# Optimization experiments

Measured on AMD Instinct MI355X. Metric: run time of the kernel, lower is better.

## Reference

```python
import jax, jax.numpy as jnp
import numpy as np

N_NODES = 50000
N_EDGES = 800000
N_GRAPHS = 16
F_IN = 128
E_DIM = 16
HID = 32
HEADS = 2
EPS_BN = 1e-5


def gatv2_conv(x, edge_index, edge_attr, Wl, bl, Wr, br, We, att, bias, heads, out_ch):
    """PyG GATv2Conv (share_weights=False, concat=True, add_self_loops=True, fill_value='mean')."""
    n = x.shape[0]
    src, dst = edge_index[0], edge_index[1]
    loop = jnp.arange(n)
    src = jnp.concatenate([src, loop])
    dst = jnp.concatenate([dst, loop])
    ea = jnp.concatenate([edge_attr, jnp.broadcast_to(edge_attr.mean(0), (n, edge_attr.shape[1]))])
    x_l = (x @ Wl + bl).reshape(n, heads, out_ch)   # source transform
    x_r = (x @ Wr + br).reshape(n, heads, out_ch)   # target transform
    e = (ea @ We).reshape(-1, heads, out_ch)
    m = jax.nn.leaky_relu(x_l[src] + x_r[dst] + e, 0.2)      # [E, H, C]
    alpha = (m * att[None]).sum(-1)                          # [E, H]
    amax = jax.ops.segment_max(alpha, dst, num_segments=n)
    ex = jnp.exp(alpha - amax[dst])
    denom = jax.ops.segment_sum(ex, dst, num_segments=n)
    alpha = ex / (denom[dst] + 1e-16)
    out = jax.ops.segment_sum(x_l[src] * alpha[..., None], dst, num_segments=n)
    return out.reshape(n, heads * out_ch) + bias


def batch_norm(x, g, b):
    mu = x.mean(0)
    var = jnp.var(x, axis=0)  # biased, as torch BatchNorm1d training mode
    return (x - mu) * jax.lax.rsqrt(var + EPS_BN) * g + b


def setup_inputs() -> dict:
    key = jax.random.key(0)
    ks = jax.random.split(key, 24)
    s = 0.1
    d1 = HID * HEADS  # 64
    inp = {
        'x': jax.random.normal(ks[0], (N_NODES, F_IN), jnp.float32),
        'edge_index': jax.random.randint(ks[1], (2, N_EDGES), 0, N_NODES),
        'edge_attr': jax.random.normal(ks[2], (N_EDGES, E_DIM), jnp.float32),
        'batch': jnp.sort(jax.random.randint(ks[3], (N_NODES,), 0, N_GRAPHS)),
        'skip1_W': jax.random.normal(ks[4], (F_IN, d1)) * s,
        'skip1_b': jnp.zeros((d1,)),
        'conv1_Wl': jax.random.normal(ks[5], (F_IN, d1)) * s,
        'conv1_bl': jnp.zeros((d1,)),
        'conv1_Wr': jax.random.normal(ks[6], (F_IN, d1)) * s,
        'conv1_br': jnp.zeros((d1,)),
        'conv1_We': jax.random.normal(ks[7], (E_DIM, d1)) * s,
        'conv1_att': jax.random.normal(ks[8], (HEADS, HID)) * s,
        'conv1_bias': jnp.zeros((d1,)),
        'bn1_g': jnp.ones((d1,)),
        'bn1_b': jnp.zeros((d1,)),
        'skip2_W': jax.random.normal(ks[9], (d1, HID)) * s,
        'skip2_b': jnp.zeros((HID,)),
        'conv2_Wl': jax.random.normal(ks[10], (d1, HID)) * s,
        'conv2_bl': jnp.zeros((HID,)),
        'conv2_Wr': jax.random.normal(ks[11], (d1, HID)) * s,
        'conv2_br': jnp.zeros((HID,)),
        'conv2_We': jax.random.normal(ks[12], (E_DIM, HID)) * s,
        'conv2_att': jax.random.normal(ks[13], (1, HID)) * s,
        'conv2_bias': jnp.zeros((HID,)),
        'bn2_g': jnp.ones((HID,)),
        'bn2_b': jnp.zeros((HID,)),
    }
    return inp


def reference(x, edge_index, edge_attr, batch,
              skip1_W, skip1_b, conv1_Wl, conv1_bl, conv1_Wr, conv1_br, conv1_We, conv1_att, conv1_bias, bn1_g, bn1_b,
              skip2_W, skip2_b, conv2_Wl, conv2_bl, conv2_Wr, conv2_br, conv2_We, conv2_att, conv2_bias, bn2_g, bn2_b):
    h_proj = x @ skip1_W + skip1_b
    h = gatv2_conv(x, edge_index, edge_attr, conv1_Wl, conv1_bl, conv1_Wr, conv1_br, conv1_We, conv1_att, conv1_bias, HEADS, HID)
    h = jax.nn.elu(batch_norm(h, bn1_g, bn1_b) + h_proj)
    h_proj = h @ skip2_W + skip2_b
    h2 = gatv2_conv(h, edge_index, edge_attr, conv2_Wl, conv2_bl, conv2_Wr, conv2_br, conv2_We, conv2_att, conv2_bias, 1, HID)
    h2 = jax.nn.elu(batch_norm(h2, bn2_g, bn2_b) + h_proj)
    ones = jnp.ones((h2.shape[0],), h2.dtype)
    counts = jax.ops.segment_sum(ones, batch, num_segments=N_GRAPHS)
    x_mean = jax.ops.segment_sum(h2, batch, num_segments=N_GRAPHS) / jnp.maximum(counts, 1.0)[:, None]
    x_max = jax.ops.segment_max(h2, batch, num_segments=N_GRAPHS)
    x_max = jnp.where(counts[:, None] > 0, x_max, 0.0)
    return jnp.concatenate([x_mean, x_max], axis=1)
```

## Files before the change

kernel.cpp:

```cpp
#include <hip/hip_runtime.h>
#include <hip/hip_bf16.h>

#define NE 800000
#define NN 50000
#define NG 16
#define ETOT (NE + NN)

typedef unsigned short u16;
typedef __attribute__((ext_vector_type(8))) short short8;
typedef __attribute__((ext_vector_type(4))) float float4v;

__device__ __forceinline__ float b2f(u16 u) {
  return __uint_as_float(((unsigned)u) << 16);
}
__device__ __forceinline__ u16 f2b(float f) {
  __hip_bfloat16 b = __float2bfloat16(f);
  return *(u16*)&b;
}
__device__ __forceinline__ void cv8(uint4 v, float* o) {
  o[0] = __uint_as_float(v.x << 16);
  o[1] = __uint_as_float(v.x & 0xFFFF0000u);
  o[2] = __uint_as_float(v.y << 16);
  o[3] = __uint_as_float(v.y & 0xFFFF0000u);
  o[4] = __uint_as_float(v.z << 16);
  o[5] = __uint_as_float(v.z & 0xFFFF0000u);
  o[6] = __uint_as_float(v.w << 16);
  o[7] = __uint_as_float(v.w & 0xFFFF0000u);
}
__device__ __forceinline__ unsigned pk2(float a, float b) {
  return (unsigned)f2b(a) | ((unsigned)f2b(b) << 16);
}
__device__ __forceinline__ unsigned f2key(float f) {
  unsigned u = __float_as_uint(f);
  return (u & 0x80000000u) ? ~u : (u | 0x80000000u);
}
__device__ __forceinline__ float key2f(unsigned k) {
  unsigned u = (k & 0x80000000u) ? (k ^ 0x80000000u) : ~k;
  return __uint_as_float(u);
}
__device__ __forceinline__ int plaus(unsigned h) {
  unsigned eh = (h >> 7) & 0xFF;
  return (h == 0) || (eh >= 100 && eh <= 140);
}
__device__ __forceinline__ float lrelu(float v) {
  return (v > 0.f) ? v : 0.2f * v;
}

__global__ __launch_bounds__(256) void k_init(uint4* __restrict__ zbase, int zcnt16,
                                              const unsigned* __restrict__ a,
                                              const unsigned* __restrict__ b,
                                              const unsigned* __restrict__ c,
                                              int* __restrict__ flags) {
  uint4 z = {0, 0, 0, 0};
  for (int i = blockIdx.x * 256 + threadIdx.x; i < zcnt16; i += gridDim.x * 256)
    zbase[i] = z;
  if (blockIdx.x != 0) return;
  __shared__ int cnt[3];
  if (threadIdx.x < 3) cnt[threadIdx.x] = 0;
  __syncthreads();
  const unsigned* arr[3] = {a, b, c};
  for (int k = 0; k < 3; k++) {
    int ok = 0;
    for (int i = threadIdx.x; i < 4096; i += 256) {
      unsigned w = arr[k][i];
      ok += (plaus(w & 0xFFFFu) && plaus(w >> 16)) ? 1 : 0;
    }
    atomicAdd(&cnt[k], ok);
  }
  __syncthreads();
  if (threadIdx.x == 0) {
    int f0 = cnt[0] > 2048, f1 = cnt[1] > 2048, f2 = cnt[2] > 2048;
    flags[0] = f0;
    flags[1] = f1;
    flags[2] = f2;
    flags[3] = f0 && f1 && f2;
  }
}

__global__ __launch_bounds__(256) void k_histcol(const int* __restrict__ ei,
                                                 const void* __restrict__ ea,
                                                 const void* __restrict__ xin,
                                                 const int* __restrict__ flg,
                                                 int* __restrict__ deg4,
                                                 float* __restrict__ mean_part,
                                                 u16* __restrict__ xh,
                                                 u16* __restrict__ xlo) {
  int gt = blockIdx.x * 256 + threadIdx.x;
  if (gt < ETOT) {
    int dst = (gt < NE) ? ei[NE + gt] : gt - NE;
    atomicAdd(&deg4[(blockIdx.x & 3) * NN + dst], 1);
  }
  bool eb = flg[2] != 0;
  int col = gt & 15;
  int row = gt >> 4;
  int rstride = (gridDim.x * 256) >> 4;
  float s = 0.f;
  if (eb) {
    const u16* p = (const u16*)ea;
    for (int e = row; e < NE; e += rstride) s += b2f(p[(size_t)e * 16 + col]);
  } else {
    const float* p = (const float*)ea;
    for (int e = row; e < NE; e += rstride) s += p[(size_t)e * 16 + col];
  }
  __shared__ float ls[256];
  ls[threadIdx.x] = s;
  __syncthreads();
  if (threadIdx.x < 16) {
    float t = 0.f;
    for (int i = threadIdx.x; i < 256; i += 16) t += ls[i];
    atomicAdd(&mean_part[(blockIdx.x & 63) * 16 + threadIdx.x], t);
  }
  if (flg[0] == 0) {
    const float4* xp4 = (const float4*)xin;
    const int nch = NN * 32;
    int stride = gridDim.x * 256;
    for (int i = gt; i < nch; i += stride) {
      float4 v = xp4[i];
      u16 h0 = f2b(v.x), h1 = f2b(v.y), h2 = f2b(v.z), h3 = f2b(v.w);
      u16 l0 = f2b(v.x - b2f(h0));
      u16 l1 = f2b(v.y - b2f(h1));
      u16 l2 = f2b(v.z - b2f(h2));
      u16 l3 = f2b(v.w - b2f(h3));
      uint2 ho, lo2;
      ho.x = (unsigned)h0 | ((unsigned)h1 << 16);
      ho.y = (unsigned)h2 | ((unsigned)h3 << 16);
      lo2.x = (unsigned)l0 | ((unsigned)l1 << 16);
      lo2.y = (unsigned)l2 | ((unsigned)l3 << 16);
      *(uint2*)(xh + (size_t)i * 4) = ho;
      *(uint2*)(xlo + (size_t)i * 4) = lo2;
    }
  }
}

template <int K, int N, int RPB>
__device__ __forceinline__ void gemm_direct(
    const void* __restrict__ W, const void* __restrict__ bb, bool wb,
    const u16* __restrict__ xh, const u16* __restrict__ xlo, bool has_lo,
    u16* __restrict__ out, int tile) {
  constexpr int CT = N / 16;
  constexpr int WPC = 4 / CT;
  constexpr int KK = K / 32;
  int lane = threadIdx.x & 63;
  int wave = threadIdx.x >> 6;
  int col = lane & 15;
  int quad = lane >> 4;
  int ct = wave % CT;
  int rt_off = wave / CT;
  short8 bh[KK], bl[KK];
#pragma unroll
  for (int kk = 0; kk < KK; kk++) {
    short8 th, tl;
#pragma unroll
    for (int j = 0; j < 8; j++) {
      int k = kk * 32 + quad * 8 + j;
      float w = wb ? b2f(((const u16*)W)[k * N + ct * 16 + col])
                   : ((const float*)W)[k * N + ct * 16 + col];
      u16 hb = f2b(w);
      th[j] = (short)hb;
      tl[j] = (short)f2b(w - b2f(hb));
    }
    bh[kk] = th;
    bl[kk] = tl;
  }
  float bias = wb ? b2f(((const u16*)bb)[ct * 16 + col])
                  : ((const float*)bb)[ct * 16 + col];
  int rt0 = tile * RPB;
  for (int i = rt_off; i < RPB; i += WPC) {
    int rt = rt0 + i;
    int row = rt * 16 + col;
    float4v acc = {0.f, 0.f, 0.f, 0.f};
#pragma unroll
    for (int kk = 0; kk < KK; kk++) {
      short8 afh = *(const short8*)(xh + (size_t)row * K + kk * 32 + quad * 8);
      acc = __builtin_amdgcn_mfma_f32_16x16x32_bf16(afh, bh[kk], acc, 0, 0, 0);
      if (has_lo) {
        short8 afl = *(const short8*)(xlo + (size_t)row * K + kk * 32 + quad * 8);
        acc = __builtin_amdgcn_mfma_f32_16x16x32_bf16(afl, bh[kk], acc, 0, 0, 0);
      }
      if (!wb)
        acc = __builtin_amdgcn_mfma_f32_16x16x32_bf16(afh, bl[kk], acc, 0, 0, 0);
    }
#pragma unroll
    for (int r = 0; r < 4; r++) {
      int orow = rt * 16 + quad * 4 + r;
      out[(size_t)orow * N + ct * 16 + col] = f2b(acc[r] + bias);
    }
  }
}

template <int K, int N, int TILES, int RPB>
__global__ __launch_bounds__(256) void k_scanlin1(
    const int* __restrict__ deg4, int* __restrict__ start, int* __restrict__ cursor,
    const float* __restrict__ mean_part, float* __restrict__ mean_sums,
    const void* __restrict__ xin, const u16* __restrict__ xh,
    const u16* __restrict__ xlo, const int* __restrict__ flg,
    const void* W0, const void* W1, const void* W2,
    const void* b0, const void* b1, const void* b2,
    u16* __restrict__ o0, u16* __restrict__ o1, u16* __restrict__ o2, int M) {
  (void)M;
  __shared__ __align__(16) int smem[512];

  if ((int)blockIdx.x == 0) {
    int t = threadIdx.x;
    if (t < 16) {
      float s = 0.f;
#pragma unroll
      for (int j = 0; j < 64; j++) s += mean_part[j * 16 + t];
      mean_sums[t] = s;
    }
    constexpr int NT = (NN + 1023) / 1024;
    int* ws = smem;
    int* tbase = ws + 256;
    int lane = t & 63;
    int wv = t >> 6;
    for (int tile = 0; tile < NT; tile++) {
      int idx = tile * 1024 + t * 4;
      int4 d = {0, 0, 0, 0};
      if (idx + 3 < NN) {
#pragma unroll
        for (int c = 0; c < 4; c++) {
          int4 dc = *(const int4*)(deg4 + c * NN + idx);
          d.x += dc.x; d.y += dc.y; d.z += dc.z; d.w += dc.w;
        }
      } else {
#pragma unroll
        for (int c = 0; c < 4; c++) {
          if (idx + 0 < NN) d.x += deg4[c * NN + idx + 0];
          if (idx + 1 < NN) d.y += deg4[c * NN + idx + 1];
          if (idx + 2 < NN) d.z += deg4[c * NN + idx + 2];
          if (idx + 3 < NN) d.w += deg4[c * NN + idx + 3];
        }
      }
      int s4 = d.x + d.y + d.z + d.w;
      int r = s4;
#pragma unroll
      for (int ofs = 1; ofs < 64; ofs <<= 1) r += __shfl_xor(r, ofs, 64);
      if (lane == 0) ws[tile * 4 + wv] = r;
    }
    __syncthreads();
    if (wv == 0) {
      int g0 = 0, g1 = 0, g2 = 0, g3 = 0;
      if (lane < NT) {
        g0 = ws[lane * 4 + 0];
        g1 = ws[lane * 4 + 1];
        g2 = ws[lane * 4 + 2];
        g3 = ws[lane * 4 + 3];
      }
      int gs = g0 + g1 + g2 + g3;
      int sc = gs;
#pragma unroll
      for (int ofs = 1; ofs < 64; ofs <<= 1) {
        int v = __shfl_up(sc, ofs, 64);
        if (lane >= ofs) sc += v;
      }
      int base = sc - gs;
      if (lane < NT) {
        tbase[lane * 4 + 0] = base;
        tbase[lane * 4 + 1] = base + g0;
        tbase[lane * 4 + 2] = base + g0 + g1;
        tbase[lane * 4 + 3] = base + g0 + g1 + g2;
      }
      if (lane == NT - 1) start[NN] = base + gs;
    }
    __syncthreads();
    for (int tile = 0; tile < NT; tile++) {
      int idx = tile * 1024 + t * 4;
      int4 d = {0, 0, 0, 0};
      if (idx + 3 < NN) {
#pragma unroll
        for (int c = 0; c < 4; c++) {
          int4 dc = *(const int4*)(deg4 + c * NN + idx);
          d.x += dc.x; d.y += dc.y; d.z += dc.z; d.w += dc.w;
        }
      } else {
#pragma unroll
        for (int c = 0; c < 4; c++) {
          if (idx + 0 < NN) d.x += deg4[c * NN + idx + 0];
          if (idx + 1 < NN) d.y += deg4[c * NN + idx + 1];
          if (idx + 2 < NN) d.z += deg4[c * NN + idx + 2];
          if (idx + 3 < NN) d.w += deg4[c * NN + idx + 3];
        }
      }
      int s4 = d.x + d.y + d.z + d.w;
      int sc = s4;
#pragma unroll
      for (int ofs = 1; ofs < 64; ofs <<= 1) {
        int v = __shfl_up(sc, ofs, 64);
        if (lane >= ofs) sc += v;
      }
      int excl = tbase[tile * 4 + wv] + (sc - s4);
      int4 st;
      st.x = excl;
      st.y = excl + d.x;
      st.z = st.y + d.y;
      st.w = st.z + d.z;
      if (idx + 3 < NN) {
        *(int4*)(start + idx) = st;
        *(int4*)(cursor + idx) = st;
      } else {
        if (idx + 0 < NN) { start[idx + 0] = st.x; cursor[idx + 0] = st.x; }
        if (idx + 1 < NN) { start[idx + 1] = st.y; cursor[idx + 1] = st.y; }
        if (idx + 2 < NN) { start[idx + 2] = st.z; cursor[idx + 2] = st.z; }
        if (idx + 3 < NN) { start[idx + 3] = st.w; cursor[idx + 3] = st.w; }
      }
    }
    return;
  }
  int lidx = blockIdx.x - 1;
  int wset = lidx / TILES;
  int tile = lidx % TILES;
  bool wb = flg[1] != 0;
  bool xb = flg[0] != 0;
  const void* W = wset == 0 ? W0 : (wset == 1 ? W1 : W2);
  const void* bb = wset == 0 ? b0 : (wset == 1 ? b1 : b2);
  u16* out = wset == 0 ? o0 : (wset == 1 ? o1 : o2);
  const u16* ah = xb ? (const u16*)xin : xh;
  gemm_direct<K, N, RPB>(W, bb, wb, ah, xlo, !xb, out, tile);
}

__global__ __launch_bounds__(256) void k_buildcsr_pay(
    const int* __restrict__ ei, const void* __restrict__ eattr,
    const int* __restrict__ flg, const float* __restrict__ mean_sums,
    int* __restrict__ cursor, int* __restrict__ csr_src,
    u16* __restrict__ ea16) {
  int e = blockIdx.x * 256 + threadIdx.x;
  if (e >= ETOT) return;
  bool eb = flg[2] != 0;
  int src, dst;
  if (e < NE) { src = ei[e]; dst = ei[NE + e]; } else { src = dst = e - NE; }
  float rec[16];
  if (e < NE) {
    if (eb) {
      const uint4* q = (const uint4*)((const u16*)eattr + (size_t)e * 16);
      cv8(q[0], rec);
      cv8(q[1], rec + 8);
    } else {
      const float* q = (const float*)eattr + (size_t)e * 16;
#pragma unroll
      for (int k = 0; k < 16; k++) rec[k] = q[k];
    }
  } else {
#pragma unroll
    for (int k = 0; k < 16; k++) rec[k] = mean_sums[k] * (1.0f / NE);
  }
  int pos = atomicAdd(&cursor[dst], 1);
  csr_src[pos] = src;
  u16 rb[16];
#pragma unroll
  for (int k = 0; k < 16; k++) rb[k] = f2b(rec[k]);
  uint4* dp = (uint4*)(ea16 + (size_t)pos * 16);
  dp[0] = *(uint4*)rb;
  dp[1] = *(uint4*)(rb + 8);
}

__global__ __launch_bounds__(256) void k_buildcsr(const int* __restrict__ ei,
                                                  int* __restrict__ cursor,
                                                  uint2* __restrict__ csr) {
  int e = blockIdx.x * 256 + threadIdx.x;
  if (e >= ETOT) return;
  int src, dst;
  if (e < NE) { src = ei[e]; dst = ei[NE + e]; } else { src = dst = e - NE; }
  int pos = atomicAdd(&cursor[dst], 1);
  uint2 r; r.x = (unsigned)src; r.y = (unsigned)e;
  csr[pos] = r;
}

__global__ __launch_bounds__(256) void k_ewgemm(
    const u16* __restrict__ ea, const int* __restrict__ flg,
    const void* We1, const void* We2,
    u16* __restrict__ ew1, u16* __restrict__ ew2) {
  bool wb = flg[1] != 0;
  int lane = threadIdx.x & 63;
  int col = lane & 15;
  int quad = lane >> 4;
  short8 b1h[4], b1l[4], b2h[2], b2l[2];
#pragma unroll
  for (int ct = 0; ct < 4; ct++) {
    short8 th, tl;
#pragma unroll
    for (int j = 0; j < 8; j++) {
      int k = quad * 8 + j;
      float w = 0.f;
      if (k < 16)
        w = wb ? b2f(((const u16*)We1)[k * 64 + ct * 16 + col])
               : ((const float*)We1)[k * 64 + ct * 16 + col];
      u16 hb = f2b(w);
      th[j] = (short)hb;
      tl[j] = (short)f2b(w - b2f(hb));
    }
    b1h[ct] = th; b1l[ct] = tl;
  }
#pragma unroll
  for (int ct = 0; ct < 2; ct++) {
    short8 th, tl;
#pragma unroll
    for (int j = 0; j < 8; j++) {
      int k = quad * 8 + j;
      float w = 0.f;
      if (k < 16)
        w = wb ? b2f(((const u16*)We2)[k * 32 + ct * 16 + col])
               : ((const float*)We2)[k * 32 + ct * 16 + col];
      u16 hb = f2b(w);
      th[j] = (short)hb;
      tl[j] = (short)f2b(w - b2f(hb));
    }
    b2h[ct] = th; b2l[ct] = tl;
  }
  int nw = (gridDim.x * 256) >> 6;
  int wid = (blockIdx.x * 256 + threadIdx.x) >> 6;
  const int NT = ETOT / 16;
  for (int rt = wid; rt < NT; rt += nw) {
    int row = rt * 16 + col;
    short8 af = {0, 0, 0, 0, 0, 0, 0, 0};
    if (quad < 2) af = *(const short8*)(ea + (size_t)row * 16 + quad * 8);
#pragma unroll
    for (int ct = 0; ct < 4; ct++) {
      float4v acc = {0.f, 0.f, 0.f, 0.f};
      acc = __builtin_amdgcn_mfma_f32_16x16x32_bf16(af, b1h[ct], acc, 0, 0, 0);
      acc = __builtin_amdgcn_mfma_f32_16x16x32_bf16(af, b1l[ct], acc, 0, 0, 0);
#pragma unroll
      for (int r = 0; r < 4; r++)
        ew1[(size_t)(rt * 16 + quad * 4 + r) * 64 + ct * 16 + col] = f2b(acc[r]);
    }
#pragma unroll
    for (int ct = 0; ct < 2; ct++) {
      float4v acc = {0.f, 0.f, 0.f, 0.f};
      acc = __builtin_amdgcn_mfma_f32_16x16x32_bf16(af, b2h[ct], acc, 0, 0, 0);
      acc = __builtin_amdgcn_mfma_f32_16x16x32_bf16(af, b2l[ct], acc, 0, 0, 0);
#pragma unroll
      for (int r = 0; r < 4; r++)
        ew2[(size_t)(rt * 16 + quad * 4 + r) * 32 + ct * 16 + col] = f2b(acc[r]);
    }
  }
}

template <int K, int N, int RPB>
__global__ __launch_bounds__(256) void k_lin3b(
    const void* __restrict__ xin, const int* __restrict__ flg,
    const void* W0, const void* W1, const void* W2,
    const void* b0, const void* b1, const void* b2,
    u16* __restrict__ o0, u16* __restrict__ o1, u16* __restrict__ o2, int M) {
  (void)M;
  bool wb = flg[1] != 0;
  const void* W = blockIdx.y == 0 ? W0 : (blockIdx.y == 1 ? W1 : W2);
  const void* bb = blockIdx.y == 0 ? b0 : (blockIdx.y == 1 ? b1 : b2);
  u16* out = blockIdx.y == 0 ? o0 : (blockIdx.y == 1 ? o1 : o2);
  gemm_direct<K, N, RPB>(W, bb, wb, (const u16*)xin, nullptr, false, out,
                         blockIdx.x);
}

__device__ __forceinline__ float dot16b(const u16* __restrict__ p,
                                        const float* __restrict__ W) {
  float ea[16];
  const uint4* q = (const uint4*)p;
  cv8(q[0], ea);
  cv8(q[1], ea + 8);
  float s = 0.f;
#pragma unroll
  for (int k = 0; k < 16; k++) s += ea[k] * W[k];
  return s;
}
__device__ __forceinline__ float dot16u(const u16* __restrict__ p,
                                        const float* __restrict__ W) {
  const uint4* q = (const uint4*)p;
  uint4 A = q[0], B = q[1];
  unsigned w0 = (unsigned)__builtin_amdgcn_readfirstlane((int)A.x);
  unsigned w1 = (unsigned)__builtin_amdgcn_readfirstlane((int)A.y);
  unsigned w2 = (unsigned)__builtin_amdgcn_readfirstlane((int)A.z);
  unsigned w3 = (unsigned)__builtin_amdgcn_readfirstlane((int)A.w);
  unsigned w4 = (unsigned)__builtin_amdgcn_readfirstlane((int)B.x);
  unsigned w5 = (unsigned)__builtin_amdgcn_readfirstlane((int)B.y);
  unsigned w6 = (unsigned)__builtin_amdgcn_readfirstlane((int)B.z);
  unsigned w7 = (unsigned)__builtin_amdgcn_readfirstlane((int)B.w);
  float s = 0.f;
  s += __uint_as_float(w0 << 16) * W[0];
  s += __uint_as_float(w0 & 0xFFFF0000u) * W[1];
  s += __uint_as_float(w1 << 16) * W[2];
  s += __uint_as_float(w1 & 0xFFFF0000u) * W[3];
  s += __uint_as_float(w2 << 16) * W[4];
  s += __uint_as_float(w2 & 0xFFFF0000u) * W[5];
  s += __uint_as_float(w3 << 16) * W[6];
  s += __uint_as_float(w3 & 0xFFFF0000u) * W[7];
  s += __uint_as_float(w4 << 16) * W[8];
  s += __uint_as_float(w4 & 0xFFFF0000u) * W[9];
  s += __uint_as_float(w5 << 16) * W[10];
  s += __uint_as_float(w5 & 0xFFFF0000u) * W[11];
  s += __uint_as_float(w6 << 16) * W[12];
  s += __uint_as_float(w6 & 0xFFFF0000u) * W[13];
  s += __uint_as_float(w7 << 16) * W[14];
  s += __uint_as_float(w7 & 0xFFFF0000u) * W[15];
  return s;
}
__device__ __forceinline__ float dot16f(const float* __restrict__ q,
                                        const float* __restrict__ W) {
  float s = 0.f;
#pragma unroll
  for (int k = 0; k < 16; k++) s += q[k] * W[k];
  return s;
}

template <int H, int C, bool PRE>
__global__ __launch_bounds__(256) void k_fusedp(
    const int* __restrict__ start, const int* __restrict__ csr_src,
    const u16* __restrict__ pay, const u16* __restrict__ ewp,
    const int* __restrict__ flg,
    const u16* __restrict__ xl, const u16* __restrict__ xr,
    const void* We, const void* att, u16* __restrict__ agg) {
  constexpr int D = H * C;
  constexpr int NPW = 64 / D;
  bool wb = flg[1] != 0;
  int lane = threadIdx.x & 63;
  int ch = lane % D;
  float Wreg[16];
  if constexpr (!PRE) {
    if (wb) {
      const u16* Wp = (const u16*)We;
#pragma unroll
      for (int k = 0; k < 16; k++) Wreg[k] = b2f(Wp[k * D + ch]);
    } else {
      const float* Wp = (const float*)We;
#pragma unroll
      for (int k = 0; k < 16; k++) Wreg[k] = Wp[k * D + ch];
    }
  }
  float attv = wb ? b2f(((const u16*)att)[ch]) : ((const float*)att)[ch];
  int wid = (blockIdx.x * 256 + threadIdx.x) >> 6;

  if constexpr (NPW == 1) {
    int node = __builtin_amdgcn_readfirstlane(wid);
    int s0 = __builtin_amdgcn_readfirstlane(start[node]);
    int s1 = __builtin_amdgcn_readfirstlane(start[node + 1]);
    float xrv = b2f(xr[(unsigned)node * D + ch]);
    float ssum = 0.f, acc = 0.f;
    int p = s0;
    for (; p + 3 < s1; p += 4) {
      int c0 = __builtin_amdgcn_readfirstlane(csr_src[p + 0]);
      int c1 = __builtin_amdgcn_readfirstlane(csr_src[p + 1]);
      int c2 = __builtin_amdgcn_readfirstlane(csr_src[p + 2]);
      int c3 = __builtin_amdgcn_readfirstlane(csr_src[p + 3]);
      float xlv0 = b2f(xl[(unsigned)c0 * D + ch]);
      float xlv1 = b2f(xl[(unsigned)c1 * D + ch]);
      float xlv2 = b2f(xl[(unsigned)c2 * D + ch]);
      float xlv3 = b2f(xl[(unsigned)c3 * D + ch]);
      float ev0, ev1, ev2, ev3;
      if constexpr (PRE) {
        ev0 = b2f(ewp[(size_t)(p + 0) * D + ch]);
        ev1 = b2f(ewp[(size_t)(p + 1) * D + ch]);
        ev2 = b2f(ewp[(size_t)(p + 2) * D + ch]);
        ev3 = b2f(ewp[(size_t)(p + 3) * D + ch]);
      } else {
        ev0 = dot16u(pay + (size_t)(p + 0) * 16, Wreg);
        ev1 = dot16u(pay + (size_t)(p + 1) * 16, Wreg);
        ev2 = dot16u(pay + (size_t)(p + 2) * 16, Wreg);
        ev3 = dot16u(pay + (size_t)(p + 3) * 16, Wreg);
      }
      float t0 = lrelu(xlv0 + xrv + ev0) * attv;
      float t1 = lrelu(xlv1 + xrv + ev1) * attv;
      float t2 = lrelu(xlv2 + xrv + ev2) * attv;
      float t3 = lrelu(xlv3 + xrv + ev3) * attv;
#pragma unroll
      for (int mk = 1; mk <= 16; mk <<= 1) {
        t0 += __shfl_xor(t0, mk, 64);
        t1 += __shfl_xor(t1, mk, 64);
        t2 += __shfl_xor(t2, mk, 64);
        t3 += __shfl_xor(t3, mk, 64);
      }
      float ex0 = __expf(t0);
      float ex1 = __expf(t1);
      float ex2 = __expf(t2);
      float ex3 = __expf(t3);
      ssum += (ex0 + ex1) + (ex2 + ex3);
      acc += ex0 * xlv0 + ex1 * xlv1;
      acc += ex2 * xlv2 + ex3 * xlv3;
    }
    for (; p < s1; ++p) {
      int c0 = __builtin_amdgcn_readfirstlane(csr_src[p]);
      float xlv = b2f(xl[(unsigned)c0 * D + ch]);
      float ev;
      if constexpr (PRE) ev = b2f(ewp[(size_t)p * D + ch]);
      else ev = dot16u(pay + (size_t)p * 16, Wreg);
      float t = lrelu(xlv + xrv + ev) * attv;
#pragma unroll
      for (int mk = 1; mk <= 16; mk <<= 1) t += __shfl_xor(t, mk, 64);
      float ex = __expf(t);
      ssum += ex;
      acc += ex * xlv;
    }
    agg[(size_t)node * D + ch] = f2b(acc / (ssum + 1e-16f));
  } else {
    int node = wid * NPW + lane / D;
    int s0 = start[node], s1 = start[node + 1];
    int deg = s1 - s0;
    int last = s1 - 1;
    int degmax = max(deg, __shfl_xor(deg, 32, 64));
    float xrv = b2f(xr[(unsigned)node * D + ch]);
    float ssum = 0.f, acc = 0.f;
    for (int i = 0; i < degmax; i += 4) {
      int p0 = min(s0 + i + 0, last);
      int p1 = min(s0 + i + 1, last);
      int p2 = min(s0 + i + 2, last);
      int p3 = min(s0 + i + 3, last);
      bool a0 = i + 0 < deg, a1 = i + 1 < deg, a2 = i + 2 < deg, a3 = i + 3 < deg;
      int c0 = csr_src[p0];
      int c1 = csr_src[p1];
      int c2 = csr_src[p2];
      int c3 = csr_src[p3];
      float xlv0 = b2f(xl[(unsigned)c0 * D + ch]);
      float xlv1 = b2f(xl[(unsigned)c1 * D + ch]);
      float xlv2 = b2f(xl[(unsigned)c2 * D + ch]);
      float xlv3 = b2f(xl[(unsigned)c3 * D + ch]);
      float ev0, ev1, ev2, ev3;
      if constexpr (PRE) {
        ev0 = b2f(ewp[(size_t)p0 * D + ch]);
        ev1 = b2f(ewp[(size_t)p1 * D + ch]);
        ev2 = b2f(ewp[(size_t)p2 * D + ch]);
        ev3 = b2f(ewp[(size_t)p3 * D + ch]);
      } else {
        ev0 = dot16b(pay + (size_t)p0 * 16, Wreg);
        ev1 = dot16b(pay + (size_t)p1 * 16, Wreg);
        ev2 = dot16b(pay + (size_t)p2 * 16, Wreg);
        ev3 = dot16b(pay + (size_t)p3 * 16, Wreg);
      }
      float t0 = lrelu(xlv0 + xrv + ev0) * attv;
      float t1 = lrelu(xlv1 + xrv + ev1) * attv;
      float t2 = lrelu(xlv2 + xrv + ev2) * attv;
      float t3 = lrelu(xlv3 + xrv + ev3) * attv;
#pragma unroll
      for (int mk = 1; mk <= 16; mk <<= 1) {
        t0 += __shfl_xor(t0, mk, 64);
        t1 += __shfl_xor(t1, mk, 64);
        t2 += __shfl_xor(t2, mk, 64);
        t3 += __shfl_xor(t3, mk, 64);
      }
      float ex0 = a0 ? __expf(t0) : 0.f;
      float ex1 = a1 ? __expf(t1) : 0.f;
      float ex2 = a2 ? __expf(t2) : 0.f;
      float ex3 = a3 ? __expf(t3) : 0.f;
      ssum += (ex0 + ex1) + (ex2 + ex3);
      acc += ex0 * xlv0 + ex1 * xlv1;
      acc += ex2 * xlv2 + ex3 * xlv3;
    }
    agg[(size_t)node * D + ch] = f2b(acc / (ssum + 1e-16f));
  }
}

template <int H, int C>
__global__ __launch_bounds__(256) void k_fusedg(
    const int* __restrict__ start, const uint2* __restrict__ csr,
    const void* __restrict__ eattr, const int* __restrict__ flg,
    const float* __restrict__ mean_sums,
    const u16* __restrict__ xl, const u16* __restrict__ xr,
    const void* We, const void* att, u16* __restrict__ agg) {
  constexpr int D = H * C;
  constexpr int NPW = 64 / D;
  bool wb = flg[1] != 0;
  bool eb = flg[2] != 0;
  int lane = threadIdx.x & 63;
  int ch = lane % D;
  float Wreg[16];
  if (wb) {
    const u16* Wp = (const u16*)We;
#pragma unroll
    for (int k = 0; k < 16; k++) Wreg[k] = b2f(Wp[k * D + ch]);
  } else {
    const float* Wp = (const float*)We;
#pragma unroll
    for (int k = 0; k < 16; k++) Wreg[k] = Wp[k * D + ch];
  }
  float attv = wb ? b2f(((const u16*)att)[ch]) : ((const float*)att)[ch];
  float ev_self = 0.f;
#pragma unroll
  for (int k = 0; k < 16; k++) ev_self += mean_sums[k] * (1.0f / NE) * Wreg[k];
  int wid = (blockIdx.x * 256 + threadIdx.x) >> 6;
  int node = wid * NPW + lane / D;
  int s0 = start[node], s1 = start[node + 1];
  int deg = s1 - s0;
  int last = s1 - 1;
  int degmax = deg;
  if constexpr (NPW == 2) degmax = max(deg, __shfl_xor(deg, 32, 64));
  float xrv = b2f(xr[(size_t)node * D + ch]);
  float ssum = 0.f, acc = 0.f;
  for (int i = 0; i < degmax; i += 2) {
    uint2 cr0 = csr[min(s0 + i, last)];
    uint2 cr1 = csr[min(s0 + i + 1, last)];
    bool a0 = i < deg, a1 = i + 1 < deg;
    float xlv0 = b2f(xl[(size_t)cr0.x * D + ch]);
    float xlv1 = b2f(xl[(size_t)cr1.x * D + ch]);
    float ev0 = cr0.y < NE ? (eb ? dot16b((const u16*)eattr + (size_t)cr0.y * 16, Wreg)
                                 : dot16f((const float*)eattr + (size_t)cr0.y * 16, Wreg))
                           : ev_self;
    float ev1 = cr1.y < NE ? (eb ? dot16b((const u16*)eattr + (size_t)cr1.y * 16, Wreg)
                                 : dot16f((const float*)eattr + (size_t)cr1.y * 16, Wreg))
                           : ev_self;
    float mv0 = xlv0 + xrv + ev0;
    float mv1 = xlv1 + xrv + ev1;
    mv0 = (mv0 > 0.f) ? mv0 : 0.2f * mv0;
    mv1 = (mv1 > 0.f) ? mv1 : 0.2f * mv1;
    float t0 = mv0 * attv, t1 = mv1 * attv;
#pragma unroll
    for (int mk = 1; mk <= 16; mk <<= 1) {
      t0 += __shfl_xor(t0, mk, 64);
      t1 += __shfl_xor(t1, mk, 64);
    }
    float ex0 = a0 ? __expf(t0) : 0.f;
    float ex1 = a1 ? __expf(t1) : 0.f;
    ssum += ex0 + ex1;
    acc += ex0 * xlv0 + ex1 * xlv1;
  }
  agg[(size_t)node * D + ch] = f2b(acc / (ssum + 1e-16f));
}

template <int D>
__global__ __launch_bounds__(256) void k_bnred(const u16* __restrict__ v,
                                               float* __restrict__ sum,
                                               float* __restrict__ sq, int M) {
  constexpr int RB = 256 / D;
  int tid = threadIdx.x;
  int c = tid % D;
  int rg = tid / D;
  float s = 0.f, q = 0.f;
  for (int r = blockIdx.x * RB + rg; r < M; r += gridDim.x * RB) {
    float x = b2f(v[(size_t)r * D + c]);
    s += x;
    q += x * x;
  }
  __shared__ float ls[256], lq[256];
  ls[tid] = s; lq[tid] = q;
  __syncthreads();
  if (tid < D) {
    float ts = 0.f, tq = 0.f;
    for (int i = tid; i < 256; i += D) { ts += ls[i]; tq += lq[i]; }
    atomicAdd(&sum[tid], ts);
    atomicAdd(&sq[tid], tq);
  }
}

template <int D>
__global__ __launch_bounds__(256) void k_bnapply(const u16* __restrict__ agg,
                                                 const u16* __restrict__ hp,
                                                 const float* __restrict__ sum,
                                                 const float* __restrict__ sq,
                                                 const void* g, const void* b,
                                                 const int* __restrict__ flg,
                                                 u16* __restrict__ out, int M) {
  bool wb = flg[1] != 0;
  int idx = blockIdx.x * 256 + threadIdx.x;
  if (idx >= M * D) return;
  int c = idx & (D - 1);
  float gc = wb ? b2f(((const u16*)g)[c]) : ((const float*)g)[c];
  float bc = wb ? b2f(((const u16*)b)[c]) : ((const float*)b)[c];
  float mu = sum[c] * (1.f / M);
  float var = fmaxf(sq[c] * (1.f / M) - mu * mu, 0.f);
  float sc = rsqrtf(var + 1e-5f) * gc;
  float v = (b2f(agg[idx]) - mu) * sc + bc + b2f(hp[idx]);
  v = v > 0.f ? v : expm1f(v);
  out[idx] = f2b(v);
}

__global__ __launch_bounds__(256) void k_poolall(
    const u16* __restrict__ agg2, const u16* __restrict__ hp2,
    const float* __restrict__ sum, const float* __restrict__ sq,
    const void* g, const void* b, const int* __restrict__ flg,
    const int* __restrict__ batch,
    float* __restrict__ pool_sum, unsigned* __restrict__ pool_maxk,
    float* __restrict__ pool_cnt, int* __restrict__ done_cnt,
    void* __restrict__ out) {
  bool wb = flg[1] != 0;
  int c = threadIdx.x & 31;
  int rg = threadIdx.x >> 5;
  float gc = wb ? b2f(((const u16*)g)[c]) : ((const float*)g)[c];
  float bc = wb ? b2f(((const u16*)b)[c]) : ((const float*)b)[c];
  float mu = sum[c] * (1.f / NN);
  float var = fmaxf(sq[c] * (1.f / NN) - mu * mu, 0.f);
  float scl = rsqrtf(var + 1e-5f) * gc;
  float sh = bc - mu * scl;

  const int NPB = 256;
  int n0 = blockIdx.x * NPB;
  int nend = min(n0 + NPB, NN);
  int cur = -1;
  float s = 0.f, mx = 0.f;
  int cnt = 0;
  for (int n = n0 + rg; n < nend; n += 8) {
    int gi = batch[n];
    float v = b2f(agg2[(size_t)n * 32 + c]) * scl + sh + b2f(hp2[(size_t)n * 32 + c]);
    v = v > 0.f ? v : expm1f(v);
    if (gi != cur) {
      if (cur >= 0) {
        atomicAdd(&pool_sum[cur * 32 + c], s);
        atomicMax(&pool_maxk[cur * 32 + c], f2key(mx));
        if (c == 0) atomicAdd(&pool_cnt[cur], (float)cnt);
      }
      cur = gi; s = 0.f; mx = -INFINITY; cnt = 0;
    }
    s += v;
    mx = fmaxf(mx, v);
    cnt++;
  }
  if (cur >= 0) {
    atomicAdd(&pool_sum[cur * 32 + c], s);
    atomicMax(&pool_maxk[cur * 32 + c], f2key(mx));
    if (c == 0) atomicAdd(&pool_cnt[cur], (float)cnt);
  }
  __threadfence();
  __syncthreads();
  __shared__ int lastblk;
  if (threadIdx.x == 0) lastblk = (atomicAdd(done_cnt, 1) == (int)gridDim.x - 1);
  __syncthreads();
  if (!lastblk) return;
  bool ob = flg[3] != 0;
  for (int idx = threadIdx.x; idx < NG * 64; idx += 256) {
    int gi = idx / 64, cc = idx % 64;
    float cntv = atomicAdd(&pool_cnt[gi], 0.f);
    float val;
    if (cc < 32) val = atomicAdd(&pool_sum[gi * 32 + cc], 0.f) / fmaxf(cntv, 1.f);
    else {
      unsigned k = atomicMax(&pool_maxk[gi * 32 + (cc - 32)], 0u);
      val = cntv > 0.f ? key2f(k) : 0.f;
    }
    if (ob) ((u16*)out)[idx] = f2b(val);
    else ((float*)out)[idx] = val;
  }
}

extern "C" void kernel_launch(void* const* d_in, const int* in_sizes, int n_in,
                              void* d_out, int out_size, void* d_ws, size_t ws_size,
                              hipStream_t stream) {
  (void)in_sizes; (void)n_in; (void)out_size;
  const void* x     = d_in[0];
  const int*  ei    = (const int*)d_in[1];
  const void* eattr = d_in[2];
  const int*  batch = (const int*)d_in[3];
  const void* skip1_W = d_in[4];
  const void* skip1_b = d_in[5];
  const void* c1_Wl = d_in[6];
  const void* c1_bl = d_in[7];
  const void* c1_Wr = d_in[8];
  const void* c1_br = d_in[9];
  const void* c1_We = d_in[10];
  const void* c1_att = d_in[11];
  const void* bn1_g = d_in[13];
  const void* bn1_b = d_in[14];
  const void* skip2_W = d_in[15];
  const void* skip2_b = d_in[16];
  const void* c2_Wl = d_in[17];
  const void* c2_bl = d_in[18];
  const void* c2_Wr = d_in[19];
  const void* c2_br = d_in[20];
  const void* c2_We = d_in[21];
  const void* c2_att = d_in[22];
  const void* bn2_g = d_in[24];
  const void* bn2_b = d_in[25];

  float* ws = (float*)d_ws;
  size_t off = 0;
  auto alloc = [&](size_t nfl) {
    float* p = ws + off;
    off += (nfl + 15) & ~(size_t)15;
    return p;
  };
  int*   flags      = (int*)alloc(16);
  float* mean_sums  = alloc(16);
  float* mean_part  = alloc(64 * 16);
  int*   deg4       = (int*)alloc((size_t)4 * NN);
  float* bnsum1     = alloc(64);
  float* bnsq1      = alloc(64);
  float* bnsum2     = alloc(32);
  float* bnsq2      = alloc(32);
  float* pool_cnt   = alloc(NG);
  float* pool_sum   = alloc(NG * 32);
  unsigned* pool_maxk = (unsigned*)alloc(NG * 32);
  int*   done_pool  = (int*)alloc(16);
  size_t zcnt16 = (off * sizeof(float)) / 16;
  u16* xh  = (u16*)alloc((size_t)NN * 64);
  u16* xlo = (u16*)alloc((size_t)NN * 64);
  size_t zoff = off;

  int* start   = (int*)alloc(NN + 1);
  int* cursor  = (int*)alloc(NN);
  int* csr_src = (int*)alloc(ETOT);
  u16* ea16    = (u16*)alloc((size_t)ETOT * 8);
  u16* ew1     = (u16*)alloc((size_t)ETOT * 32);
  u16* ew2     = (u16*)alloc((size_t)ETOT * 16);
  uint2* csr = nullptr;
  u16* xl1 = (u16*)alloc((size_t)NN * 32);
  u16* xr1 = (u16*)alloc((size_t)NN * 32);
  u16* hp1 = (u16*)alloc((size_t)NN * 32);
  u16* agg = (u16*)alloc((size_t)NN * 32);
  int tier = 0;
  if (off * sizeof(float) > ws_size) {
    tier = 1;
    off = zoff;
    start   = (int*)alloc(NN + 1);
    cursor  = (int*)alloc(NN);
    csr_src = (int*)alloc(ETOT);
    ea16    = (u16*)alloc((size_t)ETOT * 8);
    ew1 = ew2 = nullptr;
    xl1 = (u16*)alloc((size_t)NN * 32);
    xr1 = (u16*)alloc((size_t)NN * 32);
    hp1 = (u16*)alloc((size_t)NN * 32);
    agg = (u16*)alloc((size_t)NN * 32);
  }
  if (tier == 1 && off * sizeof(float) > ws_size) {
    tier = 2;
    off = zoff;
    start   = (int*)alloc(NN + 1);
    cursor  = (int*)alloc(NN);
    csr     = (uint2*)alloc((size_t)ETOT * 2);
    ea16    = nullptr;
    xl1 = (u16*)alloc((size_t)NN * 32);
    xr1 = (u16*)alloc((size_t)NN * 32);
    hp1 = (u16*)alloc((size_t)NN * 32);
    agg = (u16*)alloc((size_t)NN * 32);
  }
  u16* h1  = xr1;
  u16* xl2 = xl1;
  u16* xr2 = xl1 + (size_t)NN * 32;
  u16* hp2 = hp1;

  int eg = (ETOT + 255) / 256;

  k_init<<<128, 256, 0, stream>>>((uint4*)d_ws, (int)zcnt16,
                                  (const unsigned*)x, (const unsigned*)skip1_W,
                                  (const unsigned*)eattr, flags);
  k_histcol<<<eg, 256, 0, stream>>>(ei, eattr, x, flags, deg4, mean_part, xh, xlo);
  k_scanlin1<128, 64, 625, 5><<<1876, 256, 0, stream>>>(
      deg4, start, cursor, mean_part, mean_sums, x, xh, xlo, flags,
      c1_Wl, c1_Wr, skip1_W, c1_bl, c1_br, skip1_b, xl1, xr1, hp1, NN);
  if (tier <= 1) {
    k_buildcsr_pay<<<eg, 256, 0, stream>>>(ei, eattr, flags, mean_sums,
                                           cursor, csr_src, ea16);
  } else {
    k_buildcsr<<<eg, 256, 0, stream>>>(ei, cursor, csr);
  }
  if (tier == 0) {
    k_ewgemm<<<1024, 256, 0, stream>>>(ea16, flags, c1_We, c2_We, ew1, ew2);
  }
  if (tier == 0) {
    k_fusedp<2, 32, true><<<NN / 4, 256, 0, stream>>>(start, csr_src, ea16, ew1,
                                                      flags, xl1, xr1, c1_We,
                                                      c1_att, agg);
  } else if (tier == 1) {
    k_fusedp<2, 32, false><<<NN / 4, 256, 0, stream>>>(start, csr_src, ea16, nullptr,
                                                       flags, xl1, xr1, c1_We,
                                                       c1_att, agg);
  } else {
    k_fusedg<2, 32><<<NN / 4, 256, 0, stream>>>(start, csr, eattr, flags, mean_sums,
                                                xl1, xr1, c1_We, c1_att, agg);
  }
  k_bnred<64><<<256, 256, 0, stream>>>(agg, bnsum1, bnsq1, NN);
  k_bnapply<64><<<(NN * 64 + 255) / 256, 256, 0, stream>>>(agg, hp1, bnsum1, bnsq1,
                                                           bn1_g, bn1_b, flags, h1, NN);
  {
    dim3 g(625, 3);
    k_lin3b<64, 32, 5><<<g, 256, 0, stream>>>(h1, flags, c2_Wl, c2_Wr, skip2_W,
                                              c2_bl, c2_br, skip2_b,
                                              xl2, xr2, hp2, NN);
  }
  if (tier == 0) {
    k_fusedp<1, 32, true><<<NN / 8, 256, 0, stream>>>(start, csr_src, ea16, ew2,
                                                      flags, xl2, xr2, c2_We,
                                                      c2_att, agg);
  } else if (tier == 1) {
    k_fusedp<1, 32, false><<<NN / 8, 256, 0, stream>>>(start, csr_src, ea16, nullptr,
                                                       flags, xl2, xr2, c2_We,
                                                       c2_att, agg);
  } else {
    k_fusedg<1, 32><<<NN / 8, 256, 0, stream>>>(start, csr, eattr, flags, mean_sums,
                                                xl2, xr2, c2_We, c2_att, agg);
  }
  k_bnred<32><<<256, 256, 0, stream>>>(agg, bnsum2, bnsq2, NN);
  k_poolall<<<(NN + 255) / 256, 256, 0, stream>>>(agg, hp2, bnsum2, bnsq2,
                                                  bn2_g, bn2_b, flags, batch,
                                                  pool_sum, pool_maxk, pool_cnt,
                                                  done_pool, d_out);
}
```

Before: 589.7 us.

## Split single-block CSR prefix scan into parallel two-pass scan kernels

The degree prefix scan used to run serially inside block 0 of the fused scan+linear kernel, walking about 49 tiles of 1024 nodes twice. It now runs as two grid-wide kernels: one computes per-tile totals (and the edge-attr mean sums), the other scans those totals and writes start/cursor for each tile. The linear GEMM becomes its own kernel. This removes the long serial tail from block 0 at the cost of two extra launches and one more pass over deg4.

```diff
diff --git a/kernel.cpp b/kernel.cpp
--- a/kernel.cpp
+++ b/kernel.cpp
@@ -132,6 +132,114 @@
   }
 }
 
+#define SCAN_NT ((NN + 1023) / 1024)
+
+__global__ __launch_bounds__(256) void k_scansum(const int* __restrict__ deg4,
+                                                 const float* __restrict__ mean_part,
+                                                 float* __restrict__ mean_sums,
+                                                 int* __restrict__ tile_tot) {
+  int t = threadIdx.x;
+  if (blockIdx.x == 0 && t < 16) {
+    float s = 0.f;
+#pragma unroll
+    for (int j = 0; j < 64; j++) s += mean_part[j * 16 + t];
+    mean_sums[t] = s;
+  }
+  int lane = t & 63;
+  int wv = t >> 6;
+  int idx = blockIdx.x * 1024 + t * 4;
+  int s4 = 0;
+  if (idx + 3 < NN) {
+#pragma unroll
+    for (int c = 0; c < 4; c++) {
+      int4 dc = *(const int4*)(deg4 + c * NN + idx);
+      s4 += dc.x + dc.y + dc.z + dc.w;
+    }
+  } else {
+#pragma unroll
+    for (int c = 0; c < 4; c++) {
+      if (idx + 0 < NN) s4 += deg4[c * NN + idx + 0];
+      if (idx + 1 < NN) s4 += deg4[c * NN + idx + 1];
+      if (idx + 2 < NN) s4 += deg4[c * NN + idx + 2];
+      if (idx + 3 < NN) s4 += deg4[c * NN + idx + 3];
+    }
+  }
+  int r = s4;
+#pragma unroll
+  for (int ofs = 1; ofs < 64; ofs <<= 1) r += __shfl_xor(r, ofs, 64);
+  __shared__ int wsum[4];
+  if (lane == 0) wsum[wv] = r;
+  __syncthreads();
+  if (t == 0) tile_tot[blockIdx.x] = wsum[0] + wsum[1] + wsum[2] + wsum[3];
+}
+
+__global__ __launch_bounds__(256) void k_scanwrite(const int* __restrict__ deg4,
+                                                   const int* __restrict__ tile_tot,
+                                                   int* __restrict__ start,
+                                                   int* __restrict__ cursor) {
+  __shared__ int sbase;
+  __shared__ int wsum[4];
+  int t = threadIdx.x;
+  int lane = t & 63;
+  int wv = t >> 6;
+  if (wv == 0) {
+    int v = (lane < SCAN_NT) ? tile_tot[lane] : 0;
+    int sc = v;
+#pragma unroll
+    for (int ofs = 1; ofs < 64; ofs <<= 1) {
+      int u = __shfl_up(sc, ofs, 64);
+      if (lane >= ofs) sc += u;
+    }
+    if (lane == (int)blockIdx.x) sbase = sc - v;
+    if (blockIdx.x == 0 && lane == SCAN_NT - 1) start[NN] = sc;
+  }
+  int idx = blockIdx.x * 1024 + t * 4;
+  int4 d = {0, 0, 0, 0};
+  if (idx + 3 < NN) {
+#pragma unroll
+    for (int c = 0; c < 4; c++) {
+      int4 dc = *(const int4*)(deg4 + c * NN + idx);
+      d.x += dc.x; d.y += dc.y; d.z += dc.z; d.w += dc.w;
+    }
+  } else {
+#pragma unroll
+    for (int c = 0; c < 4; c++) {
+      if (idx + 0 < NN) d.x += deg4[c * NN + idx + 0];
+      if (idx + 1 < NN) d.y += deg4[c * NN + idx + 1];
+      if (idx + 2 < NN) d.z += deg4[c * NN + idx + 2];
+      if (idx + 3 < NN) d.w += deg4[c * NN + idx + 3];
+    }
+  }
+  int s4 = d.x + d.y + d.z + d.w;
+  int sc = s4;
+#pragma unroll
+  for (int ofs = 1; ofs < 64; ofs <<= 1) {
+    int v = __shfl_up(sc, ofs, 64);
+    if (lane >= ofs) sc += v;
+  }
+  if (lane == 63) wsum[wv] = sc;
+  __syncthreads();
+  int wbase = 0;
+#pragma unroll
+  for (int w = 0; w < 4; w++)
+    if (w < wv) wbase += wsum[w];
+  int excl = sbase + wbase + (sc - s4);
+  int4 st;
+  st.x = excl;
+  st.y = excl + d.x;
+  st.z = st.y + d.y;
+  st.w = st.z + d.z;
+  if (idx + 3 < NN) {
+    *(int4*)(start + idx) = st;
+    *(int4*)(cursor + idx) = st;
+  } else {
+    if (idx + 0 < NN) { start[idx + 0] = st.x; cursor[idx + 0] = st.x; }
+    if (idx + 1 < NN) { start[idx + 1] = st.y; cursor[idx + 1] = st.y; }
+    if (idx + 2 < NN) { start[idx + 2] = st.z; cursor[idx + 2] = st.z; }
+    if (idx + 3 < NN) { start[idx + 3] = st.w; cursor[idx + 3] = st.w; }
+  }
+}
+
 template <int K, int N, int RPB>
 __device__ __forceinline__ void gemm_direct(
     const void* __restrict__ W, const void* __restrict__ bb, bool wb,
@@ -189,124 +297,13 @@
 }
 
 template <int K, int N, int TILES, int RPB>
-__global__ __launch_bounds__(256) void k_scanlin1(
-    const int* __restrict__ deg4, int* __restrict__ start, int* __restrict__ cursor,
-    const float* __restrict__ mean_part, float* __restrict__ mean_sums,
+__global__ __launch_bounds__(256) void k_lin1(
     const void* __restrict__ xin, const u16* __restrict__ xh,
     const u16* __restrict__ xlo, const int* __restrict__ flg,
     const void* W0, const void* W1, const void* W2,
     const void* b0, const void* b1, const void* b2,
-    u16* __restrict__ o0, u16* __restrict__ o1, u16* __restrict__ o2, int M) {
-  (void)M;
-  __shared__ __align__(16) int smem[512];
-
-  if ((int)blockIdx.x == 0) {
-    int t = threadIdx.x;
-    if (t < 16) {
-      float s = 0.f;
-#pragma unroll
-      for (int j = 0; j < 64; j++) s += mean_part[j * 16 + t];
-      mean_sums[t] = s;
-    }
-    constexpr int NT = (NN + 1023) / 1024;
-    int* ws = smem;
-    int* tbase = ws + 256;
-    int lane = t & 63;
-    int wv = t >> 6;
-    for (int tile = 0; tile < NT; tile++) {
-      int idx = tile * 1024 + t * 4;
-      int4 d = {0, 0, 0, 0};
-      if (idx + 3 < NN) {
-#pragma unroll
-        for (int c = 0; c < 4; c++) {
-          int4 dc = *(const int4*)(deg4 + c * NN + idx);
-          d.x += dc.x; d.y += dc.y; d.z += dc.z; d.w += dc.w;
-        }
-      } else {
-#pragma unroll
-        for (int c = 0; c < 4; c++) {
-          if (idx + 0 < NN) d.x += deg4[c * NN + idx + 0];
-          if (idx + 1 < NN) d.y += deg4[c * NN + idx + 1];
-          if (idx + 2 < NN) d.z += deg4[c * NN + idx + 2];
-          if (idx + 3 < NN) d.w += deg4[c * NN + idx + 3];
-        }
-      }
-      int s4 = d.x + d.y + d.z + d.w;
-      int r = s4;
-#pragma unroll
-      for (int ofs = 1; ofs < 64; ofs <<= 1) r += __shfl_xor(r, ofs, 64);
-      if (lane == 0) ws[tile * 4 + wv] = r;
-    }
-    __syncthreads();
-    if (wv == 0) {
-      int g0 = 0, g1 = 0, g2 = 0, g3 = 0;
-      if (lane < NT) {
-        g0 = ws[lane * 4 + 0];
-        g1 = ws[lane * 4 + 1];
-        g2 = ws[lane * 4 + 2];
-        g3 = ws[lane * 4 + 3];
-      }
-      int gs = g0 + g1 + g2 + g3;
-      int sc = gs;
-#pragma unroll
-      for (int ofs = 1; ofs < 64; ofs <<= 1) {
-        int v = __shfl_up(sc, ofs, 64);
-        if (lane >= ofs) sc += v;
-      }
-      int base = sc - gs;
-      if (lane < NT) {
-        tbase[lane * 4 + 0] = base;
-        tbase[lane * 4 + 1] = base + g0;
-        tbase[lane * 4 + 2] = base + g0 + g1;
-        tbase[lane * 4 + 3] = base + g0 + g1 + g2;
-      }
-      if (lane == NT - 1) start[NN] = base + gs;
-    }
-    __syncthreads();
-    for (int tile = 0; tile < NT; tile++) {
-      int idx = tile * 1024 + t * 4;
-      int4 d = {0, 0, 0, 0};
-      if (idx + 3 < NN) {
-#pragma unroll
-        for (int c = 0; c < 4; c++) {
-          int4 dc = *(const int4*)(deg4 + c * NN + idx);
-          d.x += dc.x; d.y += dc.y; d.z += dc.z; d.w += dc.w;
-        }
-      } else {
-#pragma unroll
-        for (int c = 0; c < 4; c++) {
-          if (idx + 0 < NN) d.x += deg4[c * NN + idx + 0];
-          if (idx + 1 < NN) d.y += deg4[c * NN + idx + 1];
-          if (idx + 2 < NN) d.z += deg4[c * NN + idx + 2];
-          if (idx + 3 < NN) d.w += deg4[c * NN + idx + 3];
-        }
-      }
-      int s4 = d.x + d.y + d.z + d.w;
-      int sc = s4;
-#pragma unroll
-      for (int ofs = 1; ofs < 64; ofs <<= 1) {
-        int v = __shfl_up(sc, ofs, 64);
-        if (lane >= ofs) sc += v;
-      }
-      int excl = tbase[tile * 4 + wv] + (sc - s4);
-      int4 st;
-      st.x = excl;
-      st.y = excl + d.x;
-      st.z = st.y + d.y;
-      st.w = st.z + d.z;
-      if (idx + 3 < NN) {
-        *(int4*)(start + idx) = st;
-        *(int4*)(cursor + idx) = st;
-      } else {
-        if (idx + 0 < NN) { start[idx + 0] = st.x; cursor[idx + 0] = st.x; }
-        if (idx + 1 < NN) { start[idx + 1] = st.y; cursor[idx + 1] = st.y; }
-        if (idx + 2 < NN) { start[idx + 2] = st.z; cursor[idx + 2] = st.z; }
-        if (idx + 3 < NN) { start[idx + 3] = st.w; cursor[idx + 3] = st.w; }
-      }
-    }
-    return;
-  }
-  int lidx = blockIdx.x - 1;
+    u16* __restrict__ o0, u16* __restrict__ o1, u16* __restrict__ o2) {
+  int lidx = blockIdx.x;
   int wset = lidx / TILES;
   int tile = lidx % TILES;
   bool wb = flg[1] != 0;
@@ -872,6 +869,7 @@
   unsigned* pool_maxk = (unsigned*)alloc(NG * 32);
   int*   done_pool  = (int*)alloc(16);
   size_t zcnt16 = (off * sizeof(float)) / 16;
+  int*   tile_tot = (int*)alloc(64);
   u16* xh  = (u16*)alloc((size_t)NN * 64);
   u16* xlo = (u16*)alloc((size_t)NN * 64);
   size_t zoff = off;
@@ -924,9 +922,11 @@
                                   (const unsigned*)x, (const unsigned*)skip1_W,
                                   (const unsigned*)eattr, flags);
   k_histcol<<<eg, 256, 0, stream>>>(ei, eattr, x, flags, deg4, mean_part, xh, xlo);
-  k_scanlin1<128, 64, 625, 5><<<1876, 256, 0, stream>>>(
-      deg4, start, cursor, mean_part, mean_sums, x, xh, xlo, flags,
-      c1_Wl, c1_Wr, skip1_W, c1_bl, c1_br, skip1_b, xl1, xr1, hp1, NN);
+  k_scansum<<<SCAN_NT, 256, 0, stream>>>(deg4, mean_part, mean_sums, tile_tot);
+  k_scanwrite<<<SCAN_NT, 256, 0, stream>>>(deg4, tile_tot, start, cursor);
+  k_lin1<128, 64, 625, 5><<<1875, 256, 0, stream>>>(
+      x, xh, xlo, flags, c1_Wl, c1_Wr, skip1_W,
+      c1_bl, c1_br, skip1_b, xl1, xr1, hp1);
   if (tier <= 1) {
     k_buildcsr_pay<<<eg, 256, 0, stream>>>(ei, eattr, flags, mean_sums,
                                            cursor, csr_src, ea16);
```

New measurement: 557.5 us. 5.5% less time.
